# Kernel tuning notes

Hardware: AMD Instinct MI355X
Metric: run time of the kernel (lower is better)

## Reference

```python
import jax, jax.numpy as jnp
import numpy as np

N_NODES = 50000
N_EDGES = 1_280_000
NODE_D = 13
EDGE_RAW_D = 1
H = 64
CONCAT_D = 2 * NODE_D + EDGE_RAW_D  # 27
NEG_SLOPE = 0.2


def _leaky(x):
    return jnp.where(x >= 0, x, NEG_SLOPE * x)


def _scatter_mean(vals, idx, num_nodes):
    # vals: [E, H]; idx: [E] int -> [num_nodes, H] mean over incident edges (0 if none)
    s = jax.ops.segment_sum(vals, idx, num_segments=num_nodes)
    cnt = jax.ops.segment_sum(jnp.ones((vals.shape[0], 1), vals.dtype), idx, num_segments=num_nodes)
    return s / jnp.maximum(cnt, 1.0)


def _conv(e, src, dst, num_nodes, w_self, b_self, w_in, w_out):
    h_self = e @ w_self + b_self
    agg_in = _scatter_mean(e, dst, num_nodes)[src]   # incoming-edge mean at src nodes
    agg_out = _scatter_mean(e, src, num_nodes)[dst]  # outgoing-edge mean at dst nodes
    return _leaky(h_self + agg_in @ w_in + agg_out @ w_out)


def setup_inputs() -> dict:
    key = jax.random.key(0)
    ks = jax.random.split(key, 24)

    def lin(k, fan_in, fan_out):
        return jax.random.normal(k, (fan_in, fan_out), jnp.float32) / np.sqrt(fan_in)

    inp = {
        'x': jax.random.normal(ks[0], (N_NODES, NODE_D), jnp.float32),
        'edge_index': jax.random.randint(ks[1], (2, N_EDGES), 0, N_NODES, jnp.int32),
        'raw_edge_attr': jax.random.normal(ks[2], (N_EDGES, EDGE_RAW_D), jnp.float32),
        'enc_w': lin(ks[3], CONCAT_D, H),
        'enc_b': jnp.zeros((H,), jnp.float32),
    }
    for i, base in zip((1, 2, 3), (4, 8, 12)):
        inp[f'w_self{i}'] = lin(ks[base], H, H)
        inp[f'b_self{i}'] = jnp.zeros((H,), jnp.float32)
        inp[f'w_in{i}'] = lin(ks[base + 1], H, H)
        inp[f'w_out{i}'] = lin(ks[base + 2], H, H)
    dims = [(H, 64), (64, 64), (64, 32), (32, 1)]
    for j, (fi, fo) in enumerate(dims, start=1):
        inp[f'mlp_w{j}'] = lin(ks[15 + j], fi, fo)
        inp[f'mlp_b{j}'] = jnp.zeros((fo,), jnp.float32)
    return inp


def reference(x, edge_index, raw_edge_attr, enc_w, enc_b,
              w_self1, b_self1, w_in1, w_out1,
              w_self2, b_self2, w_in2, w_out2,
              w_self3, b_self3, w_in3, w_out3,
              mlp_w1, mlp_b1, mlp_w2, mlp_b2, mlp_w3, mlp_b3, mlp_w4, mlp_b4):
    num_nodes = x.shape[0]
    src, dst = edge_index[0], edge_index[1]
    edge_attr = jnp.concatenate([x[src], x[dst], raw_edge_attr], axis=-1)  # [E, 27]
    h = _leaky(edge_attr @ enc_w + enc_b)
    h = _conv(h, src, dst, num_nodes, w_self1, b_self1, w_in1, w_out1)
    h = _conv(h, src, dst, num_nodes, w_self2, b_self2, w_in2, w_out2)
    h = _conv(h, src, dst, num_nodes, w_self3, b_self3, w_in3, w_out3)
    h = _leaky(h @ mlp_w1 + mlp_b1)
    h = _leaky(h @ mlp_w2 + mlp_b2)
    h = _leaky(h @ mlp_w3 + mlp_b3)
    return (h @ mlp_w4 + mlp_b4).squeeze(-1)  # [E]
```

## Files before the change

### kernel.cpp

```cpp
#include <hip/hip_runtime.h>


#define NN 50000
#define NNP 50048
#define NE 1280000
#define LDP 72
#define NB 196
#define NTILES 782
#define CAP 64

#define WAVES 2
#define EDGE_ITERS 4
#define EDGE_BLOCKS 2500
#define ENC_ITERS 4
#define ENC_BLOCKS 2500

typedef unsigned int   u32;
typedef unsigned short u16;
typedef __attribute__((ext_vector_type(8))) short  short8;
typedef __attribute__((ext_vector_type(4))) float  floatx4;

#define MFMA16(a, b, c) __builtin_amdgcn_mfma_f32_16x16x32_bf16(a, b, c, 0, 0, 0)

__device__ __forceinline__ float lrelu(float x) { return fmaxf(x, 0.2f * x); }
__device__ __forceinline__ float bf2f(u16 u) { return __uint_as_float(((u32)u) << 16); }
__device__ __forceinline__ u16 f2bf(float f) {
    u32 b = __float_as_uint(f);
    return (u16)((b + 0x7FFFu + ((b >> 16) & 1u)) >> 16);
}
__device__ __forceinline__ u32 f2bf2(float lo, float hi) {
    u32 r;
    asm("v_cvt_pk_bf16_f32 %0, %1, %2" : "=v"(r) : "v"(lo), "v"(hi));
    return r;
}
__device__ __forceinline__ void ub2(u32 w, float& lo, float& hi) {
    lo = __uint_as_float(w << 16);
    hi = __uint_as_float(w & 0xFFFF0000u);
}

__device__ __forceinline__ short8 bfragP(const float* __restrict__ W, int ld, int n, int k0) {
    short8 b;
#pragma unroll
    for (int j = 0; j < 8; ++j) {
        const int p = k0 + j;
        const int k = (p & 3) * 16 + (p >> 2);
        b[j] = (short)f2bf(W[k * ld + n]);
    }
    return b;
}

__device__ __forceinline__ void mm_tile(const u16* __restrict__ tb,
                                        const short8 wf[2][4],
                                        floatx4 acc[4][4], int c16, int q4) {
#pragma unroll
    for (int mt = 0; mt < 4; ++mt) {
        const short8 a0 = *(const short8*)(tb + (mt * 16 + c16) * LDP + q4 * 8);
        const short8 a1 = *(const short8*)(tb + (mt * 16 + c16) * LDP + 32 + q4 * 8);
#pragma unroll
        for (int nt = 0; nt < 4; ++nt) {
            acc[mt][nt] = MFMA16(a0, wf[0][nt], acc[mt][nt]);
            acc[mt][nt] = MFMA16(a1, wf[1][nt], acc[mt][nt]);
        }
    }
}

__global__ void __launch_bounds__(256)
k_prep(const float* __restrict__ x, u16* __restrict__ xb)
{
    const int n = blockIdx.x * 256 + threadIdx.x;
    if (n >= NN) return;
    float f[13];
#pragma unroll
    for (int j = 0; j < 13; ++j) f[j] = x[n * 13 + j];
    uint4 p0, p1;
    p0.x = f2bf2(f[0],  f[1]);  p0.y = f2bf2(f[2],  f[3]);
    p0.z = f2bf2(f[4],  f[5]);  p0.w = f2bf2(f[6],  f[7]);
    p1.x = f2bf2(f[8],  f[9]);  p1.y = f2bf2(f[10], f[11]);
    p1.z = f2bf2(f[12], 0.0f);  p1.w = 0u;
    *(uint4*)(xb + (size_t)n * 16)     = p0;
    *(uint4*)(xb + (size_t)n * 16 + 8) = p1;
}

__global__ void __launch_bounds__(128)
k_enc(const u16* __restrict__ xb, const int* __restrict__ ei,
      const float* __restrict__ raw, const float* __restrict__ wenc,
      const float* __restrict__ benc, u16* __restrict__ hm,
      int* __restrict__ cnt_in, int* __restrict__ cnt_out,
      int* __restrict__ csr_in, int* __restrict__ csr_out)
{
    __shared__ int sidx[WAVES][64], didx[WAVES][64];
    const int w = threadIdx.x >> 6, lane = threadIdx.x & 63;
    const int c16 = lane & 15, q4 = lane >> 4;

    short8 wf[4];
    float bias[4];
#pragma unroll
    for (int nt = 0; nt < 4; ++nt) {
        short8 b;
#pragma unroll
        for (int j = 0; j < 8; ++j) {
            const int p = q4 * 8 + j;
            int row;
            if (p < 13)                 row = p;
            else if (p == 13)           row = 26;
            else if (p >= 16 && p < 29) row = 13 + (p - 16);
            else                        row = -1;
            b[j] = (short)(row >= 0 ? f2bf(wenc[row * 64 + nt * 16 + c16]) : 0);
        }
        wf[nt] = b;
        bias[nt] = benc[nt * 16 + c16];
    }

    for (int it = 0; it < ENC_ITERS; ++it) {
        const int tileId = (it * ENC_BLOCKS + blockIdx.x) * WAVES + w;
        const int e0 = tileId * 64;

        const int ms = ei[e0 + lane];
        const int md = ei[NE + e0 + lane];
        sidx[w][lane] = ms;
        didx[w][lane] = md;

        const int eidx = e0 + lane;
        const int p = atomicAdd(&cnt_out[ms], 1);
        if (p < CAP) csr_out[ms * CAP + p] = eidx;
        const int q = atomicAdd(&cnt_in[md], 1);
        if (q < CAP) csr_in[md * CAP + q] = eidx;

#pragma unroll
        for (int mt = 0; mt < 4; ++mt) {
            const int arow = mt * 16 + c16;
            const int* nbase = (q4 < 2) ? sidx[w] : didx[w];
            const int node = nbase[arow];
            short8 a = *(const short8*)(xb + (size_t)node * 16 + (q4 & 1) * 8);
            const float rv = raw[e0 + arow];
            if (q4 == 1) a[5] = (short)(u16)f2bf2(rv, 0.0f);

            floatx4 acc[4];
#pragma unroll
            for (int nt = 0; nt < 4; ++nt) acc[nt] = (floatx4)(0.0f);
#pragma unroll
            for (int nt = 0; nt < 4; ++nt) acc[nt] = MFMA16(a, wf[nt], acc[nt]);
#pragma unroll
            for (int r = 0; r < 4; ++r) {
                const int rowi = mt * 16 + q4 * 4 + r;
                uint2 pkt;
                pkt.x = f2bf2(lrelu(acc[0][r] + bias[0]), lrelu(acc[1][r] + bias[1]));
                pkt.y = f2bf2(lrelu(acc[2][r] + bias[2]), lrelu(acc[3][r] + bias[3]));
                *(uint2*)(hm + (size_t)(e0 + rowi) * 64 + c16 * 4) = pkt;
            }
        }
    }
}

__global__ void __launch_bounds__(256)
k_mean(const u16* __restrict__ hm,
       const int* __restrict__ cnt_in, const int* __restrict__ csr_in,
       const int* __restrict__ cnt_out, const int* __restrict__ csr_out,
       u16* __restrict__ m_in, u16* __restrict__ m_out)
{
    const int w = threadIdx.x >> 6, lane = threadIdx.x & 63;
    const int node = blockIdx.x * 4 + w;
    const int rg = lane >> 3;
    const int co = (lane & 7) * 8;

    for (int pass = 0; pass < 2; ++pass) {
        const int* cnt = pass ? cnt_out : cnt_in;
        const int* csr = pass ? csr_out : csr_in;
        u16* mp        = pass ? m_out : m_in;

        const int deg = min(cnt[node], CAP);
        const int b0 = node * CAP, b1 = b0 + deg;
        float fa[8], fb[8];
#pragma unroll
        for (int c = 0; c < 8; ++c) { fa[c] = 0.f; fb[c] = 0.f; }

        int j = b0;
        for (; j + 16 <= b1; j += 16) {
            const int ea = csr[j + rg];
            const int eb = csr[j + 8 + rg];
            const uint4 va = *(const uint4*)(hm + (size_t)ea * 64 + co);
            const uint4 vb = *(const uint4*)(hm + (size_t)eb * 64 + co);
            float l0, h0, l1, h1, l2, h2, l3, h3;
            ub2(va.x, l0, h0); ub2(va.y, l1, h1); ub2(va.z, l2, h2); ub2(va.w, l3, h3);
            fa[0] += l0; fa[1] += h0; fa[2] += l1; fa[3] += h1;
            fa[4] += l2; fa[5] += h2; fa[6] += l3; fa[7] += h3;
            ub2(vb.x, l0, h0); ub2(vb.y, l1, h1); ub2(vb.z, l2, h2); ub2(vb.w, l3, h3);
            fb[0] += l0; fb[1] += h0; fb[2] += l1; fb[3] += h1;
            fb[4] += l2; fb[5] += h2; fb[6] += l3; fb[7] += h3;
        }
        for (; j < b1; j += 8) {
            const int jj = j + rg;
            const int idx = jj < b1 ? jj : b0;
            const float fl = jj < b1 ? 1.f : 0.f;
            const int e = csr[idx];
            const uint4 v = *(const uint4*)(hm + (size_t)e * 64 + co);
            float l0, h0, l1, h1, l2, h2, l3, h3;
            ub2(v.x, l0, h0); ub2(v.y, l1, h1); ub2(v.z, l2, h2); ub2(v.w, l3, h3);
            fa[0] += fl * l0; fa[1] += fl * h0; fa[2] += fl * l1; fa[3] += fl * h1;
            fa[4] += fl * l2; fa[5] += fl * h2; fa[6] += fl * l3; fa[7] += fl * h3;
        }
#pragma unroll
        for (int c = 0; c < 8; ++c) fa[c] += fb[c];
#pragma unroll
        for (int d = 8; d < 64; d <<= 1)
#pragma unroll
            for (int c = 0; c < 8; ++c) fa[c] += __shfl_xor(fa[c], d, 64);

        const float inv = 1.0f / (float)(deg > 0 ? deg : 1);
        if (lane < 8) {
            uint4 p;
            p.x = f2bf2(fa[0] * inv, fa[1] * inv);
            p.y = f2bf2(fa[2] * inv, fa[3] * inv);
            p.z = f2bf2(fa[4] * inv, fa[5] * inv);
            p.w = f2bf2(fa[6] * inv, fa[7] * inv);
            *(uint4*)(mp + (size_t)node * 64 + lane * 8) = p;
        }
    }
}

__global__ void __launch_bounds__(256)
k_nodemm(u16* t_in, u16* t_out,
         const float* __restrict__ w_in, const float* __restrict__ w_out)
{
    const int w = threadIdx.x >> 6, lane = threadIdx.x & 63;
    const int c16 = lane & 15, q4 = lane >> 4;
    const int tileId = blockIdx.x * 4 + w;
    if (tileId >= NTILES) return;
    const int n0 = tileId * 64;

    for (int pass = 0; pass < 2; ++pass) {
        u16* tp         = pass ? t_out : t_in;
        const float* wp = pass ? w_out : w_in;

        short8 wf[2][4];
#pragma unroll
        for (int ks = 0; ks < 2; ++ks)
#pragma unroll
            for (int nt = 0; nt < 4; ++nt)
                wf[ks][nt] = bfragP(wp, 64, nt * 16 + c16, ks * 32 + q4 * 8);

#pragma unroll
        for (int mt = 0; mt < 4; ++mt) {
            const short8* ap = (const short8*)(tp + (size_t)(n0 + mt * 16 + c16) * 64 + q4 * 8);
            const short8 a0 = ap[0];
            const short8 a1 = ap[4];
            floatx4 acc[4];
#pragma unroll
            for (int nt = 0; nt < 4; ++nt) acc[nt] = (floatx4)(0.0f);
#pragma unroll
            for (int nt = 0; nt < 4; ++nt) {
                acc[nt] = MFMA16(a0, wf[0][nt], acc[nt]);
                acc[nt] = MFMA16(a1, wf[1][nt], acc[nt]);
            }
#pragma unroll
            for (int r = 0; r < 4; ++r) {
                const int node = n0 + mt * 16 + q4 * 4 + r;
                if (node < NN) {
                    uint2 pkt;
                    pkt.x = f2bf2(acc[0][r], acc[1][r]);
                    pkt.y = f2bf2(acc[2][r], acc[3][r]);
                    *(uint2*)(tp + (size_t)node * 64 + c16 * 4) = pkt;
                }
            }
        }
    }
}

__global__ void __launch_bounds__(128, 3)
k_edge(const float* __restrict__ wself, const float* __restrict__ bself,
       const u16* __restrict__ t_in, const u16* __restrict__ t_out,
       const int* __restrict__ ei, u16* __restrict__ hm)
{
    __shared__ int sidx[WAVES][64], didx[WAVES][64];
    const int w = threadIdx.x >> 6, lane = threadIdx.x & 63;
    const int c16 = lane & 15, q4 = lane >> 4;

    short8 wf[2][4];
    float bias[4];
#pragma unroll
    for (int ks = 0; ks < 2; ++ks)
#pragma unroll
        for (int nt = 0; nt < 4; ++nt)
            wf[ks][nt] = bfragP(wself, 64, nt * 16 + c16, ks * 32 + q4 * 8);
#pragma unroll
    for (int nt = 0; nt < 4; ++nt) bias[nt] = bself[nt * 16 + c16];

    int e0 = (blockIdx.x * WAVES + w) * 64;
    sidx[w][lane] = ei[e0 + lane];
    didx[w][lane] = ei[NE + e0 + lane];
    short8 pa0[4], pa1[4];
#pragma unroll
    for (int mt = 0; mt < 4; ++mt) {
        const short8* ap = (const short8*)(hm + (size_t)(e0 + mt * 16 + c16) * 64 + q4 * 8);
        pa0[mt] = ap[0]; pa1[mt] = ap[4];
    }

#pragma unroll 1
    for (int it = 0; it < EDGE_ITERS; ++it) {
        const bool more = (it + 1 < EDGE_ITERS);
        const int e0n = (((it + 1) * EDGE_BLOCKS + blockIdx.x) * WAVES + w) * 64;
        int sN = 0, dN = 0;
        if (more) { sN = ei[e0n + lane]; dN = ei[NE + e0n + lane]; }

#pragma unroll
        for (int mt = 0; mt < 4; ++mt) {
            floatx4 acc[4];
#pragma unroll
            for (int nt = 0; nt < 4; ++nt) acc[nt] = (floatx4)(0.0f);
#pragma unroll
            for (int nt = 0; nt < 4; ++nt) {
                acc[nt] = MFMA16(pa0[mt], wf[0][nt], acc[nt]);
                acc[nt] = MFMA16(pa1[mt], wf[1][nt], acc[nt]);
            }
            if (more) {
                const short8* ap = (const short8*)(hm + (size_t)(e0n + mt * 16 + c16) * 64 + q4 * 8);
                pa0[mt] = ap[0]; pa1[mt] = ap[4];
            }
            float tv[4][4], uv[4][4];
#pragma unroll
            for (int r = 0; r < 4; ++r) {
                const int s = sidx[w][mt * 16 + q4 * 4 + r];
                const uint2 v = *(const uint2*)(t_in + (size_t)s * 64 + c16 * 4);
                ub2(v.x, tv[r][0], tv[r][1]); ub2(v.y, tv[r][2], tv[r][3]);
            }
#pragma unroll
            for (int r = 0; r < 4; ++r) {
                const int d = didx[w][mt * 16 + q4 * 4 + r];
                const uint2 v = *(const uint2*)(t_out + (size_t)d * 64 + c16 * 4);
                ub2(v.x, uv[r][0], uv[r][1]); ub2(v.y, uv[r][2], uv[r][3]);
            }
#pragma unroll
            for (int r = 0; r < 4; ++r) {
                const int row = mt * 16 + q4 * 4 + r;
                const float v0 = lrelu(acc[0][r] + bias[0] + tv[r][0] + uv[r][0]);
                const float v1 = lrelu(acc[1][r] + bias[1] + tv[r][1] + uv[r][1]);
                const float v2 = lrelu(acc[2][r] + bias[2] + tv[r][2] + uv[r][2]);
                const float v3 = lrelu(acc[3][r] + bias[3] + tv[r][3] + uv[r][3]);
                uint2 pkt; pkt.x = f2bf2(v0, v1); pkt.y = f2bf2(v2, v3);
                *(uint2*)(hm + (size_t)(e0 + row) * 64 + c16 * 4) = pkt;
            }
        }
        if (more) { sidx[w][lane] = sN; didx[w][lane] = dN; }
        e0 = e0n;
    }
}

__global__ void __launch_bounds__(128, 2)
k_edge_mlp(const float* __restrict__ wself, const float* __restrict__ bself,
           const u16* __restrict__ t_in, const u16* __restrict__ t_out,
           const int* __restrict__ ei, const u16* __restrict__ hm,
           const float* __restrict__ w1, const float* __restrict__ b1,
           const float* __restrict__ w2, const float* __restrict__ b2,
           const float* __restrict__ w3, const float* __restrict__ b3,
           const float* __restrict__ w4, const float* __restrict__ b4,
           float* __restrict__ out)
{
    __shared__ alignas(16) u16 tile[WAVES][64 * LDP];
    __shared__ int sidx[WAVES][64], didx[WAVES][64];
    const int w = threadIdx.x >> 6, lane = threadIdx.x & 63;
    const int c16 = lane & 15, q4 = lane >> 4;

    short8 wfS[2][4], wf1[2][4], wf2[2][4], wf3[2][2];
    float bS[4], bv1[4], bv2[4], bv3[2];
#pragma unroll
    for (int ks = 0; ks < 2; ++ks) {
#pragma unroll
        for (int nt = 0; nt < 4; ++nt) {
            wfS[ks][nt] = bfragP(wself, 64, nt * 16 + c16, ks * 32 + q4 * 8);
            wf1[ks][nt] = bfragP(w1,    64, nt * 16 + c16, ks * 32 + q4 * 8);
            wf2[ks][nt] = bfragP(w2,    64, nt * 16 + c16, ks * 32 + q4 * 8);
        }
#pragma unroll
        for (int nt = 0; nt < 2; ++nt)
            wf3[ks][nt] = bfragP(w3, 32, nt * 16 + c16, ks * 32 + q4 * 8);
    }
#pragma unroll
    for (int nt = 0; nt < 4; ++nt) { bS[nt] = bself[nt*16+c16]; bv1[nt] = b1[nt*16+c16]; bv2[nt] = b2[nt*16+c16]; }
#pragma unroll
    for (int nt = 0; nt < 2; ++nt) bv3[nt] = b3[nt * 16 + c16];
    const float w4a = w4[c16], w4b = w4[16 + c16], b4v = b4[0];

    int e0 = (blockIdx.x * WAVES + w) * 64;
    sidx[w][lane] = ei[e0 + lane];
    didx[w][lane] = ei[NE + e0 + lane];
    short8 pa0[4], pa1[4];
#pragma unroll
    for (int mt = 0; mt < 4; ++mt) {
        const short8* ap = (const short8*)(hm + (size_t)(e0 + mt * 16 + c16) * 64 + q4 * 8);
        pa0[mt] = ap[0]; pa1[mt] = ap[4];
    }

#pragma unroll 1
    for (int it = 0; it < EDGE_ITERS; ++it) {
        const bool more = (it + 1 < EDGE_ITERS);
        const int e0n = (((it + 1) * EDGE_BLOCKS + blockIdx.x) * WAVES + w) * 64;
        int sN = 0, dN = 0;
        if (more) { sN = ei[e0n + lane]; dN = ei[NE + e0n + lane]; }

#pragma unroll
        for (int mt = 0; mt < 4; ++mt) {
            floatx4 acc[4];
#pragma unroll
            for (int nt = 0; nt < 4; ++nt) acc[nt] = (floatx4)(0.0f);
#pragma unroll
            for (int nt = 0; nt < 4; ++nt) {
                acc[nt] = MFMA16(pa0[mt], wfS[0][nt], acc[nt]);
                acc[nt] = MFMA16(pa1[mt], wfS[1][nt], acc[nt]);
            }
            if (more) {
                const short8* ap = (const short8*)(hm + (size_t)(e0n + mt * 16 + c16) * 64 + q4 * 8);
                pa0[mt] = ap[0]; pa1[mt] = ap[4];
            }
            float tv[4][4], uv[4][4];
#pragma unroll
            for (int r = 0; r < 4; ++r) {
                const int s = sidx[w][mt * 16 + q4 * 4 + r];
                const uint2 v = *(const uint2*)(t_in + (size_t)s * 64 + c16 * 4);
                ub2(v.x, tv[r][0], tv[r][1]); ub2(v.y, tv[r][2], tv[r][3]);
            }
#pragma unroll
            for (int r = 0; r < 4; ++r) {
                const int d = didx[w][mt * 16 + q4 * 4 + r];
                const uint2 v = *(const uint2*)(t_out + (size_t)d * 64 + c16 * 4);
                ub2(v.x, uv[r][0], uv[r][1]); ub2(v.y, uv[r][2], uv[r][3]);
            }
#pragma unroll
            for (int r = 0; r < 4; ++r) {
                const int row = mt * 16 + q4 * 4 + r;
                const float v0 = lrelu(acc[0][r] + bS[0] + tv[r][0] + uv[r][0]);
                const float v1 = lrelu(acc[1][r] + bS[1] + tv[r][1] + uv[r][1]);
                const float v2 = lrelu(acc[2][r] + bS[2] + tv[r][2] + uv[r][2]);
                const float v3 = lrelu(acc[3][r] + bS[3] + tv[r][3] + uv[r][3]);
                uint2 pkt; pkt.x = f2bf2(v0, v1); pkt.y = f2bf2(v2, v3);
                *(uint2*)(tile[w] + row * LDP + c16 * 4) = pkt;
            }
        }
        if (more) { sidx[w][lane] = sN; didx[w][lane] = dN; }

        floatx4 acc[4][4];
#pragma unroll
        for (int mt = 0; mt < 4; ++mt)
#pragma unroll
            for (int nt = 0; nt < 4; ++nt) acc[mt][nt] = (floatx4)(0.0f);
        mm_tile(tile[w], wf1, acc, c16, q4);
#pragma unroll
        for (int mt = 0; mt < 4; ++mt)
#pragma unroll
            for (int r = 0; r < 4; ++r) {
                const int row = mt * 16 + q4 * 4 + r;
                uint2 pkt;
                pkt.x = f2bf2(lrelu(acc[mt][0][r] + bv1[0]), lrelu(acc[mt][1][r] + bv1[1]));
                pkt.y = f2bf2(lrelu(acc[mt][2][r] + bv1[2]), lrelu(acc[mt][3][r] + bv1[3]));
                *(uint2*)(tile[w] + row * LDP + c16 * 4) = pkt;
            }

#pragma unroll
        for (int mt = 0; mt < 4; ++mt)
#pragma unroll
            for (int nt = 0; nt < 4; ++nt) acc[mt][nt] = (floatx4)(0.0f);
        mm_tile(tile[w], wf2, acc, c16, q4);
#pragma unroll
        for (int mt = 0; mt < 4; ++mt)
#pragma unroll
            for (int r = 0; r < 4; ++r) {
                const int row = mt * 16 + q4 * 4 + r;
                uint2 pkt;
                pkt.x = f2bf2(lrelu(acc[mt][0][r] + bv2[0]), lrelu(acc[mt][1][r] + bv2[1]));
                pkt.y = f2bf2(lrelu(acc[mt][2][r] + bv2[2]), lrelu(acc[mt][3][r] + bv2[3]));
                *(uint2*)(tile[w] + row * LDP + c16 * 4) = pkt;
            }

        floatx4 a3[4][2];
#pragma unroll
        for (int mt = 0; mt < 4; ++mt)
#pragma unroll
            for (int nt = 0; nt < 2; ++nt) a3[mt][nt] = (floatx4)(0.0f);
#pragma unroll
        for (int mt = 0; mt < 4; ++mt) {
            const short8 a0 = *(const short8*)(tile[w] + (mt * 16 + c16) * LDP + q4 * 8);
            const short8 a1 = *(const short8*)(tile[w] + (mt * 16 + c16) * LDP + 32 + q4 * 8);
#pragma unroll
            for (int nt = 0; nt < 2; ++nt) {
                a3[mt][nt] = MFMA16(a0, wf3[0][nt], a3[mt][nt]);
                a3[mt][nt] = MFMA16(a1, wf3[1][nt], a3[mt][nt]);
            }
        }
#pragma unroll
        for (int mt = 0; mt < 4; ++mt)
#pragma unroll
            for (int r = 0; r < 4; ++r) {
                float p = lrelu(a3[mt][0][r] + bv3[0]) * w4a
                        + lrelu(a3[mt][1][r] + bv3[1]) * w4b;
                p += __shfl_xor(p, 1, 64);
                p += __shfl_xor(p, 2, 64);
                p += __shfl_xor(p, 4, 64);
                p += __shfl_xor(p, 8, 64);
                if (c16 == 0) out[e0 + mt * 16 + q4 * 4 + r] = p + b4v;
            }
        e0 = e0n;
    }
}

extern "C" void kernel_launch(void* const* d_in, const int* in_sizes, int n_in,
                              void* d_out, int out_size, void* d_ws, size_t ws_size,
                              hipStream_t stream)
{
    const float* x      = (const float*)d_in[0];
    const int*   ei     = (const int*)  d_in[1];
    const float* raw    = (const float*)d_in[2];
    const float* wenc   = (const float*)d_in[3];
    const float* benc   = (const float*)d_in[4];
    const float* wself1 = (const float*)d_in[5];
    const float* bself1 = (const float*)d_in[6];
    const float* win1   = (const float*)d_in[7];
    const float* wout1  = (const float*)d_in[8];
    const float* wself2 = (const float*)d_in[9];
    const float* bself2 = (const float*)d_in[10];
    const float* win2   = (const float*)d_in[11];
    const float* wout2  = (const float*)d_in[12];
    const float* wself3 = (const float*)d_in[13];
    const float* bself3 = (const float*)d_in[14];
    const float* win3   = (const float*)d_in[15];
    const float* wout3  = (const float*)d_in[16];
    const float* w1 = (const float*)d_in[17]; const float* b1 = (const float*)d_in[18];
    const float* w2 = (const float*)d_in[19]; const float* b2 = (const float*)d_in[20];
    const float* w3 = (const float*)d_in[21]; const float* b3 = (const float*)d_in[22];
    const float* w4 = (const float*)d_in[23]; const float* b4 = (const float*)d_in[24];

    u16*   t_in    = (u16*)d_ws;
    u16*   t_out   = t_in + (size_t)NNP * 64;
    int*   cnt_in  = (int*)(t_out + (size_t)NNP * 64);
    int*   cnt_out = cnt_in + NN;
    int*   csr_in  = cnt_out + NN;
    int*   csr_out = csr_in + (size_t)NN * CAP;
    u16*   hm      = (u16*)(csr_out + (size_t)NN * CAP);

    u16*   xb      = t_in;

    hipMemsetAsync(cnt_in, 0, (size_t)2 * NN * sizeof(int), stream);

    k_prep<<<NB, 256, 0, stream>>>(x, xb);

    k_enc<<<ENC_BLOCKS, 128, 0, stream>>>(xb, ei, raw, wenc, benc, hm,
                                          cnt_in, cnt_out, csr_in, csr_out);

    for (int layer = 0; layer < 3; ++layer) {
        const float* wi = layer == 0 ? win1  : layer == 1 ? win2  : win3;
        const float* wo = layer == 0 ? wout1 : layer == 1 ? wout2 : wout3;
        k_mean<<<NN / 4, 256, 0, stream>>>(hm, cnt_in, csr_in, cnt_out, csr_out,
                                           t_in, t_out);
        k_nodemm<<<NB, 256, 0, stream>>>(t_in, t_out, wi, wo);
        if (layer == 0)
            k_edge<<<EDGE_BLOCKS, 128, 0, stream>>>(wself1, bself1, t_in, t_out, ei, hm);
        else if (layer == 1)
            k_edge<<<EDGE_BLOCKS, 128, 0, stream>>>(wself2, bself2, t_in, t_out, ei, hm);
        else
            k_edge_mlp<<<EDGE_BLOCKS, 128, 0, stream>>>(wself3, bself3, t_in, t_out, ei, hm,
                                                        w1, b1, w2, b2, w3, b3, w4, b4,
                                                        (float*)d_out);
    }
}
```

Baseline: 745.8 us.

## Split CSR fill into node-range-partitioned blocks alongside encoder blocks

Moves the adjacency-list atomic fill out of the encoder loop into separate blocks of the same launch. Each fill block handles a slice of edges for one of 8 node-range classes, so each class's atomics and CSR writes land in a narrower memory region, which may improve L2 locality. The cost is that every edge index is read 8 times, and the fill blocks contend with the encoder MFMA blocks for the GPU.

After: 741.3 us. Within noise of the previous version (-0.6%).

```diff
diff --git a/kernel.cpp b/kernel.cpp
--- a/kernel.cpp
+++ b/kernel.cpp
@@ -8,12 +8,14 @@
 #define NB 196
 #define NTILES 782
 #define CAP 64
+#define NPX 6250
 
 #define WAVES 2
 #define EDGE_ITERS 4
 #define EDGE_BLOCKS 2500
 #define ENC_ITERS 4
 #define ENC_BLOCKS 2500
+#define FILL_BLOCKS 10000
 
 typedef unsigned int   u32;
 typedef unsigned short u16;
@@ -82,13 +84,39 @@
 }
 
 __global__ void __launch_bounds__(128)
-k_enc(const u16* __restrict__ xb, const int* __restrict__ ei,
-      const float* __restrict__ raw, const float* __restrict__ wenc,
-      const float* __restrict__ benc, u16* __restrict__ hm,
-      int* __restrict__ cnt_in, int* __restrict__ cnt_out,
-      int* __restrict__ csr_in, int* __restrict__ csr_out)
+k_enc_fill(const u16* __restrict__ xb, const int* __restrict__ ei,
+           const float* __restrict__ raw, const float* __restrict__ wenc,
+           const float* __restrict__ benc, u16* __restrict__ hm,
+           int* __restrict__ cnt_in, int* __restrict__ cnt_out,
+           int* __restrict__ csr_in, int* __restrict__ csr_out)
 {
     __shared__ int sidx[WAVES][64], didx[WAVES][64];
+
+    if (blockIdx.x >= ENC_BLOCKS) {
+        const int cls   = blockIdx.x & 7;
+        const int slice = (blockIdx.x - ENC_BLOCKS) >> 3;
+        const int base  = (slice * 128 + threadIdx.x) * 8;
+        const int lo = cls * NPX, hi = lo + NPX;
+        int s[8], d[8];
+#pragma unroll
+        for (int k = 0; k < 8; ++k) s[k] = ei[base + k];
+#pragma unroll
+        for (int k = 0; k < 8; ++k) d[k] = ei[NE + base + k];
+#pragma unroll
+        for (int k = 0; k < 8; ++k)
+            if (s[k] >= lo && s[k] < hi) {
+                const int p = atomicAdd(&cnt_out[s[k]], 1);
+                if (p < CAP) csr_out[s[k] * CAP + p] = base + k;
+            }
+#pragma unroll
+        for (int k = 0; k < 8; ++k)
+            if (d[k] >= lo && d[k] < hi) {
+                const int q = atomicAdd(&cnt_in[d[k]], 1);
+                if (q < CAP) csr_in[d[k] * CAP + q] = base + k;
+            }
+        return;
+    }
+
     const int w = threadIdx.x >> 6, lane = threadIdx.x & 63;
     const int c16 = lane & 15, q4 = lane >> 4;
 
@@ -115,16 +143,8 @@
         const int tileId = (it * ENC_BLOCKS + blockIdx.x) * WAVES + w;
         const int e0 = tileId * 64;
 
-        const int ms = ei[e0 + lane];
-        const int md = ei[NE + e0 + lane];
-        sidx[w][lane] = ms;
-        didx[w][lane] = md;
-
-        const int eidx = e0 + lane;
-        const int p = atomicAdd(&cnt_out[ms], 1);
-        if (p < CAP) csr_out[ms * CAP + p] = eidx;
-        const int q = atomicAdd(&cnt_in[md], 1);
-        if (q < CAP) csr_in[md * CAP + q] = eidx;
+        sidx[w][lane] = ei[e0 + lane];
+        didx[w][lane] = ei[NE + e0 + lane];
 
 #pragma unroll
         for (int mt = 0; mt < 4; ++mt) {
@@ -541,8 +561,8 @@
 
     k_prep<<<NB, 256, 0, stream>>>(x, xb);
 
-    k_enc<<<ENC_BLOCKS, 128, 0, stream>>>(xb, ei, raw, wenc, benc, hm,
-                                          cnt_in, cnt_out, csr_in, csr_out);
+    k_enc_fill<<<ENC_BLOCKS + FILL_BLOCKS, 128, 0, stream>>>(
+        xb, ei, raw, wenc, benc, hm, cnt_in, cnt_out, csr_in, csr_out);
 
     for (int layer = 0; layer < 3; ++layer) {
         const float* wi = layer == 0 ? win1  : layer == 1 ? win2  : win3;
```
